# Kernel optimization log

Hardware: AMD Instinct MI355X
Metric: run time of the kernel (lower is better)

The kernel has to match this reference:

```python
import jax, jax.numpy as jnp
import numpy as np


def setup_inputs() -> dict:
    key = jax.random.key(0)
    ks = jax.random.split(key, 8)
    B, I, H = 4096, 2048, 2048
    C = I + H
    s = 1.0 / np.sqrt(C)
    return {
        "x": jax.random.normal(ks[0], (B, I), jnp.float32),
        "h": jax.random.normal(ks[1], (B, H), jnp.float32),
        "W_update": jax.random.normal(ks[2], (H, C), jnp.float32) * s,
        "b_update": jax.random.normal(ks[3], (H,), jnp.float32) * s,
        "W_select": jax.random.normal(ks[4], (H, C), jnp.float32) * s,
        "b_select": jax.random.normal(ks[5], (H,), jnp.float32) * s,
        "W_predict": jax.random.normal(ks[6], (H, C), jnp.float32) * s,
        "b_predict": jax.random.normal(ks[7], (H,), jnp.float32) * s,
    }


def reference(x, h, W_update, b_update, W_select, b_select, W_predict, b_predict):
    # combined = [x, h]  -> [B, I+H]
    combined = jnp.concatenate([x, h], axis=1)
    to_update = jax.nn.sigmoid(combined @ W_update.T + b_update)  # [B, H]
    to_select = jax.nn.sigmoid(combined @ W_select.T + b_select)  # [B, H]
    updated = h * to_update
    new_combined = jnp.concatenate([x, updated], axis=1)
    predictions = jnp.tanh(new_combined @ W_predict.T + b_predict)
    selected = predictions * to_select
    h_new = h * (1.0 - to_select) + selected
    return h_new
```

## Files before the change

### kernel.cpp

```cpp
#include <hip/hip_runtime.h>
#include <stdint.h>

#define IDIM 2048
#define HDIM 2048
#define CDIM 4096
#define BDIM 4096
#define KDIM 4096

typedef float f32x4 __attribute__((ext_vector_type(4)));
typedef short s16x8 __attribute__((ext_vector_type(8)));
typedef unsigned short u16;
typedef u16 u16x8 __attribute__((ext_vector_type(8)));

__device__ __forceinline__ u16 f2bf(float f) {
    union { float f; uint32_t u; } v; v.f = f;
    uint32_t r = v.u + 0x7fffu + ((v.u >> 16) & 1u);
    return (u16)(r >> 16);
}

__device__ __forceinline__ void gload_lds16(const void* g, void* l) {
    __builtin_amdgcn_global_load_lds(
        (__attribute__((address_space(1))) void*)g,
        (__attribute__((address_space(3))) void*)l,
        16, 0, 0);
}

__global__ void cvt_bf16_kernel(const float* __restrict__ src, u16* __restrict__ dst,
                                int ngroups) {
    int i = blockIdx.x * blockDim.x + threadIdx.x;
    if (i >= ngroups) return;
    const float4* s4 = (const float4*)src;
    float4 v0 = s4[2 * i], v1 = s4[2 * i + 1];
    u16x8 o;
    o[0] = f2bf(v0.x); o[1] = f2bf(v0.y); o[2] = f2bf(v0.z); o[3] = f2bf(v0.w);
    o[4] = f2bf(v1.x); o[5] = f2bf(v1.y); o[6] = f2bf(v1.z); o[7] = f2bf(v1.w);
    ((u16x8*)dst)[i] = o;
}

__global__ void pack_combined_kernel(const float* __restrict__ x, const float* __restrict__ h,
                                     u16* __restrict__ comb, u16* __restrict__ newc) {
    int i = blockIdx.x * blockDim.x + threadIdx.x;
    if (i >= BDIM * (CDIM / 8)) return;
    int b = i >> 9;
    int c = (i & 511) * 8;
    const float* src = (c < IDIM) ? (x + (size_t)b * IDIM + c)
                                  : (h + (size_t)b * HDIM + (c - IDIM));
    float4 v0 = ((const float4*)src)[0], v1 = ((const float4*)src)[1];
    u16x8 o;
    o[0] = f2bf(v0.x); o[1] = f2bf(v0.y); o[2] = f2bf(v0.z); o[3] = f2bf(v0.w);
    o[4] = f2bf(v1.x); o[5] = f2bf(v1.y); o[6] = f2bf(v1.z); o[7] = f2bf(v1.w);
    *(u16x8*)(comb + (size_t)b * CDIM + c) = o;
    if (c < IDIM) *(u16x8*)(newc + (size_t)b * CDIM + c) = o;
}

__global__ void gemm_bt1(const u16* __restrict__ A, const u16* __restrict__ Bm,
                         const float* __restrict__ h,
                         const float* __restrict__ bias0, const float* __restrict__ bias1,
                         float* __restrict__ Sout, u16* __restrict__ newc) {
    constexpr int BM = 128, BK = 64;
    const int tid  = threadIdx.x;
    const int lane = tid & 63;
    const int wave = tid >> 6;
    const int wr = wave >> 1, wc = wave & 1;
    const int bm = blockIdx.y * BM;
    const int bn = blockIdx.x * BM;

    __shared__ __align__(16) u16 lA[BM * BK];
    __shared__ __align__(16) u16 lB[BM * BK];

    f32x4 acc[4][4] = {};

    const int srow = wave * 32 + (lane >> 3);
    const int sg   = (lane & 7) ^ (lane >> 3);

    auto stage = [&](int k0) {
        #pragma unroll
        for (int i = 0; i < 4; ++i) {
            const int r = srow + i * 8;
            gload_lds16(A  + (size_t)(bm + r) * KDIM + k0 + sg * 8,
                        &lA[(wave * 32 + i * 8) * 64]);
            gload_lds16(Bm + (size_t)(bn + r) * KDIM + k0 + sg * 8,
                        &lB[(wave * 32 + i * 8) * 64]);
        }
    };

    stage(0);
    constexpr int NT = KDIM / BK;
    for (int kt = 0; kt < NT; ++kt) {
        __syncthreads();
        #pragma unroll
        for (int ks = 0; ks < 2; ++ks) {
            s16x8 af[4], bfr[4];
            #pragma unroll
            for (int m = 0; m < 4; ++m) {
                const int row = wr * 64 + m * 16 + (lane & 15);
                const int j   = ks * 4 + (lane >> 4);
                af[m] = *(const s16x8*)&lA[row * 64 + ((j ^ (row & 7)) << 3)];
            }
            #pragma unroll
            for (int n = 0; n < 4; ++n) {
                const int row = wc * 64 + n * 16 + (lane & 15);
                const int j   = ks * 4 + (lane >> 4);
                bfr[n] = *(const s16x8*)&lB[row * 64 + ((j ^ (row & 7)) << 3)];
            }
            #pragma unroll
            for (int m = 0; m < 4; ++m)
                #pragma unroll
                for (int n = 0; n < 4; ++n)
                    acc[m][n] = __builtin_amdgcn_mfma_f32_16x16x32_bf16(
                        af[m], bfr[n], acc[m][n], 0, 0, 0);
        }
        __syncthreads();
        if (kt + 1 < NT) stage((kt + 1) * BK);
    }

    #pragma unroll
    for (int m = 0; m < 4; ++m) {
        const int r0 = bm + wr * 64 + m * 16 + ((lane >> 4) << 2);
        #pragma unroll
        for (int n = 0; n < 4; ++n) {
            const int col = bn + wc * 64 + n * 16 + (lane & 15);
            #pragma unroll
            for (int j = 0; j < 4; ++j) {
                const int r = r0 + j;
                const float v = acc[m][n][j];
                const float bv = (col < HDIM) ? bias0[col] : bias1[col - HDIM];
                const float sgm = 1.0f / (1.0f + __expf(-(v + bv)));
                if (col < HDIM) {
                    const float hv = h[(size_t)r * HDIM + col];
                    newc[(size_t)r * CDIM + IDIM + col] = f2bf(hv * sgm);
                } else {
                    Sout[(size_t)r * HDIM + (col - HDIM)] = sgm;
                }
            }
        }
    }
}

__global__ void gemm_bt2(const u16* __restrict__ A, const u16* __restrict__ Bm,
                         const float* __restrict__ h,
                         const float* __restrict__ bias0,
                         float* __restrict__ Sout) {
    constexpr int BM = 128, BN = 64, BK = 64;
    const int tid  = threadIdx.x;
    const int lane = tid & 63;
    const int wave = tid >> 6;
    const int wr = wave >> 1, wc = wave & 1;
    const int bm = blockIdx.y * BM;
    const int bn = blockIdx.x * BN;

    __shared__ __align__(16) u16 lA[BM * BK];
    __shared__ __align__(16) u16 lB[BN * BK];

    f32x4 acc[4][2] = {};

    const int sg = (lane & 7) ^ (lane >> 3);

    auto stage = [&](int k0) {
        #pragma unroll
        for (int i = 0; i < 4; ++i) {
            const int r = wave * 32 + i * 8 + (lane >> 3);
            gload_lds16(A + (size_t)(bm + r) * KDIM + k0 + sg * 8,
                        &lA[(wave * 32 + i * 8) * 64]);
        }
        #pragma unroll
        for (int i = 0; i < 2; ++i) {
            const int r = wave * 16 + i * 8 + (lane >> 3);
            gload_lds16(Bm + (size_t)(bn + r) * KDIM + k0 + sg * 8,
                        &lB[(wave * 16 + i * 8) * 64]);
        }
    };

    stage(0);
    constexpr int NT = KDIM / BK;
    for (int kt = 0; kt < NT; ++kt) {
        __syncthreads();
        #pragma unroll
        for (int ks = 0; ks < 2; ++ks) {
            s16x8 af[4], bfr[2];
            #pragma unroll
            for (int m = 0; m < 4; ++m) {
                const int row = wr * 64 + m * 16 + (lane & 15);
                const int j   = ks * 4 + (lane >> 4);
                af[m] = *(const s16x8*)&lA[row * 64 + ((j ^ (row & 7)) << 3)];
            }
            #pragma unroll
            for (int n = 0; n < 2; ++n) {
                const int row = wc * 32 + n * 16 + (lane & 15);
                const int j   = ks * 4 + (lane >> 4);
                bfr[n] = *(const s16x8*)&lB[row * 64 + ((j ^ (row & 7)) << 3)];
            }
            #pragma unroll
            for (int m = 0; m < 4; ++m)
                #pragma unroll
                for (int n = 0; n < 2; ++n)
                    acc[m][n] = __builtin_amdgcn_mfma_f32_16x16x32_bf16(
                        af[m], bfr[n], acc[m][n], 0, 0, 0);
        }
        __syncthreads();
        if (kt + 1 < NT) stage((kt + 1) * BK);
    }

    #pragma unroll
    for (int m = 0; m < 4; ++m) {
        const int r0 = bm + wr * 64 + m * 16 + ((lane >> 4) << 2);
        #pragma unroll
        for (int n = 0; n < 2; ++n) {
            const int col = bn + wc * 32 + n * 16 + (lane & 15);
            #pragma unroll
            for (int j = 0; j < 4; ++j) {
                const int r = r0 + j;
                const float p = tanhf(acc[m][n][j] + bias0[col]);
                const size_t idx = (size_t)r * HDIM + col;
                const float s  = Sout[idx];
                const float hv = h[idx];
                Sout[idx] = hv * (1.0f - s) + p * s;
            }
        }
    }
}

extern "C" void kernel_launch(void* const* d_in, const int* in_sizes, int n_in,
                              void* d_out, int out_size, void* d_ws, size_t ws_size,
                              hipStream_t stream) {
    (void)in_sizes; (void)n_in; (void)out_size; (void)ws_size;
    const float* x  = (const float*)d_in[0];
    const float* h  = (const float*)d_in[1];
    const float* Wu = (const float*)d_in[2];
    const float* bu = (const float*)d_in[3];
    const float* Ws = (const float*)d_in[4];
    const float* bs = (const float*)d_in[5];
    const float* Wp = (const float*)d_in[6];
    const float* bp = (const float*)d_in[7];
    float* out = (float*)d_out;

    u16* comb  = (u16*)d_ws;
    u16* newc  = comb  + (size_t)BDIM * CDIM;
    u16* wpack = newc  + (size_t)BDIM * CDIM;
    u16* wpred = wpack + (size_t)2 * HDIM * CDIM;

    const int WG = 256;
    const int wgrp = (HDIM * CDIM) / 8;
    cvt_bf16_kernel<<<wgrp / WG, WG, 0, stream>>>(Wu, wpack, wgrp);
    cvt_bf16_kernel<<<wgrp / WG, WG, 0, stream>>>(Ws, wpack + (size_t)HDIM * CDIM, wgrp);
    cvt_bf16_kernel<<<wgrp / WG, WG, 0, stream>>>(Wp, wpred, wgrp);
    const int cgrp = (BDIM * CDIM) / 8;
    pack_combined_kernel<<<cgrp / WG, WG, 0, stream>>>(x, h, comb, newc);

    gemm_bt1<<<dim3(CDIM / 128, BDIM / 128), 256, 0, stream>>>(
        comb, wpack, h, bu, bs, out, newc);
    gemm_bt2<<<dim3(HDIM / 64, BDIM / 128), 256, 0, stream>>>(
        newc, wpred, h, bp, out);
}
```

Baseline: 286.8 us.

## Rewrite first GEMM as 256x256 double-buffered 8-wave pipelined kernel

Replaces the 128x128 single-buffered gate GEMM with a 256x256 tile, 512-thread kernel that double-buffers LDS and splits each k-tile into four phases. Each phase interleaves async global->LDS prefetch of the next tile with MFMA on quadrants, using explicit waitcnt, barriers and setprio. It aims to hide load latency and raise arithmetic intensity for the largest GEMM. In exchange it needs 128 KB of LDS per block and more registers, which limits occupancy, and the hand-tuned waitcnt values must match the issue order exactly.

```diff
diff --git a/kernel.cpp b/kernel.cpp
--- a/kernel.cpp
+++ b/kernel.cpp
@@ -53,85 +53,148 @@
     if (c < IDIM) *(u16x8*)(newc + (size_t)b * CDIM + c) = o;
 }
 
-__global__ void gemm_bt1(const u16* __restrict__ A, const u16* __restrict__ Bm,
-                         const float* __restrict__ h,
-                         const float* __restrict__ bias0, const float* __restrict__ bias1,
-                         float* __restrict__ Sout, u16* __restrict__ newc) {
-    constexpr int BM = 128, BK = 64;
+__global__ __launch_bounds__(512, 2) void gemm8p(
+        const u16* __restrict__ A, const u16* __restrict__ Bm,
+        const float* __restrict__ h,
+        const float* __restrict__ bias0, const float* __restrict__ bias1,
+        float* __restrict__ Sout, u16* __restrict__ newc) {
+    constexpr int NT = KDIM / 64;
+
     const int tid  = threadIdx.x;
     const int lane = tid & 63;
     const int wave = tid >> 6;
-    const int wr = wave >> 1, wc = wave & 1;
-    const int bm = blockIdx.y * BM;
-    const int bn = blockIdx.x * BM;
-
-    __shared__ __align__(16) u16 lA[BM * BK];
-    __shared__ __align__(16) u16 lB[BM * BK];
-
-    f32x4 acc[4][4] = {};
-
-    const int srow = wave * 32 + (lane >> 3);
-    const int sg   = (lane & 7) ^ (lane >> 3);
-
-    auto stage = [&](int k0) {
-        #pragma unroll
-        for (int i = 0; i < 4; ++i) {
-            const int r = srow + i * 8;
-            gload_lds16(A  + (size_t)(bm + r) * KDIM + k0 + sg * 8,
-                        &lA[(wave * 32 + i * 8) * 64]);
-            gload_lds16(Bm + (size_t)(bn + r) * KDIM + k0 + sg * 8,
-                        &lB[(wave * 32 + i * 8) * 64]);
-        }
-    };
-
-    stage(0);
-    constexpr int NT = KDIM / BK;
-    for (int kt = 0; kt < NT; ++kt) {
-        __syncthreads();
-        #pragma unroll
-        for (int ks = 0; ks < 2; ++ks) {
-            s16x8 af[4], bfr[4];
-            #pragma unroll
-            for (int m = 0; m < 4; ++m) {
-                const int row = wr * 64 + m * 16 + (lane & 15);
-                const int j   = ks * 4 + (lane >> 4);
-                af[m] = *(const s16x8*)&lA[row * 64 + ((j ^ (row & 7)) << 3)];
-            }
-            #pragma unroll
-            for (int n = 0; n < 4; ++n) {
-                const int row = wc * 64 + n * 16 + (lane & 15);
-                const int j   = ks * 4 + (lane >> 4);
-                bfr[n] = *(const s16x8*)&lB[row * 64 + ((j ^ (row & 7)) << 3)];
-            }
-            #pragma unroll
-            for (int m = 0; m < 4; ++m)
-                #pragma unroll
-                for (int n = 0; n < 4; ++n)
-                    acc[m][n] = __builtin_amdgcn_mfma_f32_16x16x32_bf16(
-                        af[m], bfr[n], acc[m][n], 0, 0, 0);
-        }
-        __syncthreads();
-        if (kt + 1 < NT) stage((kt + 1) * BK);
-    }
-
-    #pragma unroll
-    for (int m = 0; m < 4; ++m) {
-        const int r0 = bm + wr * 64 + m * 16 + ((lane >> 4) << 2);
-        #pragma unroll
-        for (int n = 0; n < 4; ++n) {
-            const int col = bn + wc * 64 + n * 16 + (lane & 15);
-            #pragma unroll
-            for (int j = 0; j < 4; ++j) {
-                const int r = r0 + j;
-                const float v = acc[m][n][j];
-                const float bv = (col < HDIM) ? bias0[col] : bias1[col - HDIM];
-                const float sgm = 1.0f / (1.0f + __expf(-(v + bv)));
-                if (col < HDIM) {
-                    const float hv = h[(size_t)r * HDIM + col];
-                    newc[(size_t)r * CDIM + IDIM + col] = f2bf(hv * sgm);
-                } else {
-                    Sout[(size_t)r * HDIM + (col - HDIM)] = sgm;
-                }
+    const int wr = wave >> 2, wc = wave & 3;
+    const int bm = blockIdx.y * 256;
+    const int bn = blockIdx.x * 256;
+
+    __shared__ __align__(16) u16 lA[2][256 * 64];
+    __shared__ __align__(16) u16 lB[2][256 * 64];
+
+    f32x4 acc[8][4] = {};
+    s16x8 af[4][2];
+    s16x8 bq[2][2][2];
+
+    const int srow = tid >> 3;
+    const int ssw  = ((tid & 7) ^ ((tid >> 3) & 7)) << 3;
+
+#define STAGE_A(NB, c, k0)                                                      \
+    gload_lds16(A + (size_t)(bm + (c) * 64 + srow) * KDIM + (k0) + ssw,         \
+                &lA[NB][((c) * 64 + wave * 8) * 64]);
+#define STAGE_B(NB, c, k0)                                                      \
+    gload_lds16(Bm + (size_t)(bn + (c) * 64 + srow) * KDIM + (k0) + ssw,        \
+                &lB[NB][((c) * 64 + wave * 8) * 64]);
+
+#define READ_A(BUF, QM)                                                         \
+    _Pragma("unroll") for (int fm = 0; fm < 4; ++fm) {                          \
+        const int row_ = wr * 64 + (QM) * 128 + fm * 16 + (lane & 15);          \
+        const int bo_ = row_ * 64; const int rx_ = row_ & 7;                    \
+        af[fm][0] = *(const s16x8*)&lA[BUF][bo_ + ((((lane >> 4)    ) ^ rx_) << 3)]; \
+        af[fm][1] = *(const s16x8*)&lA[BUF][bo_ + ((((lane >> 4) + 4) ^ rx_) << 3)]; \
+    }
+#define READ_B(BUF, QN)                                                         \
+    _Pragma("unroll") for (int nf = 0; nf < 2; ++nf) {                          \
+        const int row_ = wc * 32 + (QN) * 128 + nf * 16 + (lane & 15);          \
+        const int bo_ = row_ * 64; const int rx_ = row_ & 7;                    \
+        bq[QN][nf][0] = *(const s16x8*)&lB[BUF][bo_ + ((((lane >> 4)    ) ^ rx_) << 3)]; \
+        bq[QN][nf][1] = *(const s16x8*)&lB[BUF][bo_ + ((((lane >> 4) + 4) ^ rx_) << 3)]; \
+    }
+#define MFMA_QUAD(QM, QN)                                                       \
+    _Pragma("unroll") for (int ks = 0; ks < 2; ++ks)                            \
+    _Pragma("unroll") for (int fm = 0; fm < 4; ++fm)                            \
+    _Pragma("unroll") for (int nf = 0; nf < 2; ++nf)                            \
+        acc[(QM) * 4 + fm][(QN) * 2 + nf] =                                     \
+            __builtin_amdgcn_mfma_f32_16x16x32_bf16(                            \
+                af[fm][ks], bq[QN][nf][ks], acc[(QM) * 4 + fm][(QN) * 2 + nf], 0, 0, 0);
+#define PHASE_MID()                                                             \
+    __builtin_amdgcn_s_barrier();                                               \
+    asm volatile("s_waitcnt lgkmcnt(0)" ::: "memory");                          \
+    __builtin_amdgcn_sched_barrier(0);                                          \
+    __builtin_amdgcn_s_setprio(1);
+#define PHASE_END(W)                                                            \
+    __builtin_amdgcn_s_setprio(0);                                              \
+    asm volatile("s_waitcnt vmcnt(" #W ")" ::: "memory");                       \
+    __builtin_amdgcn_s_barrier();
+#define PHASE_END_NOWAIT()                                                      \
+    __builtin_amdgcn_s_setprio(0);                                              \
+    __builtin_amdgcn_s_barrier();
+
+#define KTILE(BUF, NB, KN, PF, W0, W1, W3)                                      \
+    {                                                                           \
+                 \
+        READ_A(BUF, 0)                                                          \
+        READ_B(BUF, 0)                                                          \
+        if (PF) { STAGE_A(NB, 0, KN); STAGE_A(NB, 1, KN); }                     \
+        asm volatile("s_waitcnt lgkmcnt(8)" ::: "memory");                      \
+        PHASE_MID();                                                            \
+        MFMA_QUAD(0, 0);                                                        \
+        PHASE_END(W0);                                                          \
+                          \
+        READ_B(BUF, 1)                                                          \
+        if (PF) { STAGE_B(NB, 0, KN); STAGE_B(NB, 1, KN); }                     \
+        PHASE_MID();                                                            \
+        MFMA_QUAD(0, 1);                                                        \
+        PHASE_END(W1);                                                          \
+                          \
+        READ_A(BUF, 1)                                                          \
+        if (PF) { STAGE_B(NB, 2, KN); STAGE_B(NB, 3, KN); }                     \
+        PHASE_MID();                                                            \
+        MFMA_QUAD(1, 1);                                                        \
+        PHASE_END_NOWAIT();                                                     \
+                              \
+        if (PF) { STAGE_A(NB, 2, KN); STAGE_A(NB, 3, KN); }                     \
+        PHASE_MID();                                                            \
+        MFMA_QUAD(1, 0);                                                        \
+        PHASE_END(W3);                                                          \
+    }
+
+    STAGE_A(0, 0, 0); STAGE_A(0, 1, 0);
+    STAGE_B(0, 0, 0); STAGE_B(0, 1, 0);
+    STAGE_B(0, 2, 0); STAGE_B(0, 3, 0);
+    STAGE_A(0, 2, 0); STAGE_A(0, 3, 0);
+    asm volatile("s_waitcnt vmcnt(4)" ::: "memory");
+    __builtin_amdgcn_s_barrier();
+
+    for (int kt = 0; kt < NT - 2; kt += 2) {
+        const int kn0 = (kt + 1) * 64;
+        const int kn1 = (kt + 2) * 64;
+        KTILE(0, 1, kn0, 1, 4, 4, 4);
+        KTILE(1, 0, kn1, 1, 4, 4, 4);
+    }
+    KTILE(0, 1, (NT - 1) * 64, 1, 4, 4, 4);
+    KTILE(1, 0, 0, 0, 2, 0, 0);
+
+#undef KTILE
+#undef READ_A
+#undef READ_B
+#undef MFMA_QUAD
+#undef PHASE_MID
+#undef PHASE_END
+#undef PHASE_END_NOWAIT
+#undef STAGE_A
+#undef STAGE_B
+
+    #pragma unroll
+    for (int qm = 0; qm < 2; ++qm)
+    #pragma unroll
+    for (int fm = 0; fm < 4; ++fm)
+    #pragma unroll
+    for (int qn = 0; qn < 2; ++qn)
+    #pragma unroll
+    for (int nf = 0; nf < 2; ++nf) {
+        const int r0  = bm + wr * 64 + qm * 128 + fm * 16 + ((lane >> 4) << 2);
+        const int col = bn + wc * 32 + qn * 128 + nf * 16 + (lane & 15);
+        const f32x4 a = acc[qm * 4 + fm][qn * 2 + nf];
+        #pragma unroll
+        for (int j = 0; j < 4; ++j) {
+            const int r = r0 + j;
+            const float v = a[j];
+            const float bv = (col < HDIM) ? bias0[col] : bias1[col - HDIM];
+            const float sgm = 1.0f / (1.0f + __expf(-(v + bv)));
+            if (col < HDIM) {
+                const float hv = h[(size_t)r * HDIM + col];
+                newc[(size_t)r * CDIM + IDIM + col] = f2bf(hv * sgm);
+            } else {
+                Sout[(size_t)r * HDIM + (col - HDIM)] = sgm;
             }
         }
     }
@@ -247,7 +310,7 @@
     const int cgrp = (BDIM * CDIM) / 8;
     pack_combined_kernel<<<cgrp / WG, WG, 0, stream>>>(x, h, comb, newc);
 
-    gemm_bt1<<<dim3(CDIM / 128, BDIM / 128), 256, 0, stream>>>(
+    gemm8p<<<dim3(CDIM / 256, BDIM / 256), 512, 0, stream>>>(
         comb, wpack, h, bu, bs, out, newc);
     gemm_bt2<<<dim3(HDIM / 64, BDIM / 128), 256, 0, stream>>>(
         newc, wpred, h, bp, out);
```

New measurement: 295.6 us. 1.03x slower.

## Merge prep conversions into one kernel, fuse Wp cast into GEMM1, retile GEMM2

Applied to the files above, without the earlier changes.

Merges the three weight-cast launches and the combined-pack launch into one prep kernel. The W_predict bf16 conversion moves into the tail of the first GEMM, with each block converting a slice after its epilogue. The second GEMM now runs 2 waves of 128 threads, each computing 64x64, with launch bounds for 3 blocks per CU. This cuts launch count and gives GEMM2 more MFMA work per LDS load, at the cost of extra tail work in GEMM1 and fewer waves per block in GEMM2.

```diff
diff --git a/kernel.cpp b/kernel.cpp
--- a/kernel.cpp
+++ b/kernel.cpp
@@ -18,6 +18,13 @@
     return (u16)(r >> 16);
 }
 
+__device__ __forceinline__ u16x8 cvt8(float4 v0, float4 v1) {
+    u16x8 o;
+    o[0] = f2bf(v0.x); o[1] = f2bf(v0.y); o[2] = f2bf(v0.z); o[3] = f2bf(v0.w);
+    o[4] = f2bf(v1.x); o[5] = f2bf(v1.y); o[6] = f2bf(v1.z); o[7] = f2bf(v1.w);
+    return o;
+}
+
 __device__ __forceinline__ void gload_lds16(const void* g, void* l) {
     __builtin_amdgcn_global_load_lds(
         (__attribute__((address_space(1))) void*)g,
@@ -25,38 +32,35 @@
         16, 0, 0);
 }
 
-__global__ void cvt_bf16_kernel(const float* __restrict__ src, u16* __restrict__ dst,
-                                int ngroups) {
+__global__ void prep_kernel(const float* __restrict__ x, const float* __restrict__ h,
+                            const float* __restrict__ Wu, const float* __restrict__ Ws,
+                            u16* __restrict__ comb, u16* __restrict__ newc,
+                            u16* __restrict__ wpack) {
+    const int WCNT = (HDIM * CDIM) / 8;
     int i = blockIdx.x * blockDim.x + threadIdx.x;
-    if (i >= ngroups) return;
-    const float4* s4 = (const float4*)src;
-    float4 v0 = s4[2 * i], v1 = s4[2 * i + 1];
-    u16x8 o;
-    o[0] = f2bf(v0.x); o[1] = f2bf(v0.y); o[2] = f2bf(v0.z); o[3] = f2bf(v0.w);
-    o[4] = f2bf(v1.x); o[5] = f2bf(v1.y); o[6] = f2bf(v1.z); o[7] = f2bf(v1.w);
-    ((u16x8*)dst)[i] = o;
-}
-
-__global__ void pack_combined_kernel(const float* __restrict__ x, const float* __restrict__ h,
-                                     u16* __restrict__ comb, u16* __restrict__ newc) {
-    int i = blockIdx.x * blockDim.x + threadIdx.x;
-    if (i >= BDIM * (CDIM / 8)) return;
-    int b = i >> 9;
-    int c = (i & 511) * 8;
-    const float* src = (c < IDIM) ? (x + (size_t)b * IDIM + c)
-                                  : (h + (size_t)b * HDIM + (c - IDIM));
-    float4 v0 = ((const float4*)src)[0], v1 = ((const float4*)src)[1];
-    u16x8 o;
-    o[0] = f2bf(v0.x); o[1] = f2bf(v0.y); o[2] = f2bf(v0.z); o[3] = f2bf(v0.w);
-    o[4] = f2bf(v1.x); o[5] = f2bf(v1.y); o[6] = f2bf(v1.z); o[7] = f2bf(v1.w);
-    *(u16x8*)(comb + (size_t)b * CDIM + c) = o;
-    if (c < IDIM) *(u16x8*)(newc + (size_t)b * CDIM + c) = o;
+    if (i < 2 * WCNT) {
+        const float* src = (i < WCNT) ? Wu : Ws;
+        const int g = (i < WCNT) ? i : i - WCNT;
+        u16* dst = wpack + (i < WCNT ? (size_t)0 : (size_t)HDIM * CDIM);
+        const float4* s4 = (const float4*)src;
+        ((u16x8*)dst)[g] = cvt8(s4[2 * g], s4[2 * g + 1]);
+    } else {
+        const int p = i - 2 * WCNT;
+        const int b = p >> 9;
+        const int c = (p & 511) * 8;
+        const float* src = (c < IDIM) ? (x + (size_t)b * IDIM + c)
+                                      : (h + (size_t)b * HDIM + (c - IDIM));
+        u16x8 o = cvt8(((const float4*)src)[0], ((const float4*)src)[1]);
+        *(u16x8*)(comb + (size_t)b * CDIM + c) = o;
+        if (c < IDIM) *(u16x8*)(newc + (size_t)b * CDIM + c) = o;
+    }
 }
 
 __global__ void gemm_bt1(const u16* __restrict__ A, const u16* __restrict__ Bm,
                          const float* __restrict__ h,
                          const float* __restrict__ bias0, const float* __restrict__ bias1,
-                         float* __restrict__ Sout, u16* __restrict__ newc) {
+                         float* __restrict__ Sout, u16* __restrict__ newc,
+                         const float* __restrict__ Wp, u16* __restrict__ wpred) {
     constexpr int BM = 128, BK = 64;
     const int tid  = threadIdx.x;
     const int lane = tid & 63;
@@ -135,40 +139,48 @@
             }
         }
     }
-}
-
-__global__ void gemm_bt2(const u16* __restrict__ A, const u16* __restrict__ Bm,
-                         const float* __restrict__ h,
-                         const float* __restrict__ bias0,
-                         float* __restrict__ Sout) {
+
+    {
+        const int bid = blockIdx.y * (CDIM / 128) + blockIdx.x;
+        const size_t base = (size_t)bid * 8192;
+        const float4* s4 = (const float4*)(Wp + base);
+        u16x8* d8 = (u16x8*)(wpred + base);
+        #pragma unroll
+        for (int t = 0; t < 4; ++t) {
+            const int g = t * 256 + tid;
+            d8[g] = cvt8(s4[2 * g], s4[2 * g + 1]);
+        }
+    }
+}
+
+__global__ __launch_bounds__(128, 3) void gemm_bt2(
+        const u16* __restrict__ A, const u16* __restrict__ Bm,
+        const float* __restrict__ h, const float* __restrict__ bias0,
+        float* __restrict__ Sout) {
     constexpr int BM = 128, BN = 64, BK = 64;
     const int tid  = threadIdx.x;
     const int lane = tid & 63;
     const int wave = tid >> 6;
-    const int wr = wave >> 1, wc = wave & 1;
     const int bm = blockIdx.y * BM;
     const int bn = blockIdx.x * BN;
 
     __shared__ __align__(16) u16 lA[BM * BK];
     __shared__ __align__(16) u16 lB[BN * BK];
 
-    f32x4 acc[4][2] = {};
-
-    const int sg = (lane & 7) ^ (lane >> 3);
+    f32x4 acc[4][4] = {};
+
+    const int srow = tid >> 3;
+    const int ssw  = ((tid & 7) ^ (srow & 7)) << 3;
 
     auto stage = [&](int k0) {
         #pragma unroll
-        for (int i = 0; i < 4; ++i) {
-            const int r = wave * 32 + i * 8 + (lane >> 3);
-            gload_lds16(A + (size_t)(bm + r) * KDIM + k0 + sg * 8,
-                        &lA[(wave * 32 + i * 8) * 64]);
-        }
-        #pragma unroll
-        for (int i = 0; i < 2; ++i) {
-            const int r = wave * 16 + i * 8 + (lane >> 3);
-            gload_lds16(Bm + (size_t)(bn + r) * KDIM + k0 + sg * 8,
-                        &lB[(wave * 16 + i * 8) * 64]);
-        }
+        for (int c = 0; c < 8; ++c)
+            gload_lds16(A + (size_t)(bm + c * 16 + srow) * KDIM + k0 + ssw,
+                        &lA[(c * 16 + wave * 8) * 64]);
+        #pragma unroll
+        for (int c = 0; c < 4; ++c)
+            gload_lds16(Bm + (size_t)(bn + c * 16 + srow) * KDIM + k0 + ssw,
+                        &lB[(c * 16 + wave * 8) * 64]);
     };
 
     stage(0);
@@ -177,23 +189,23 @@
         __syncthreads();
         #pragma unroll
         for (int ks = 0; ks < 2; ++ks) {
-            s16x8 af[4], bfr[2];
+            s16x8 af[4], bfr[4];
             #pragma unroll
             for (int m = 0; m < 4; ++m) {
-                const int row = wr * 64 + m * 16 + (lane & 15);
+                const int row = wave * 64 + m * 16 + (lane & 15);
                 const int j   = ks * 4 + (lane >> 4);
                 af[m] = *(const s16x8*)&lA[row * 64 + ((j ^ (row & 7)) << 3)];
             }
             #pragma unroll
-            for (int n = 0; n < 2; ++n) {
-                const int row = wc * 32 + n * 16 + (lane & 15);
+            for (int n = 0; n < 4; ++n) {
+                const int row = n * 16 + (lane & 15);
                 const int j   = ks * 4 + (lane >> 4);
                 bfr[n] = *(const s16x8*)&lB[row * 64 + ((j ^ (row & 7)) << 3)];
             }
             #pragma unroll
             for (int m = 0; m < 4; ++m)
                 #pragma unroll
-                for (int n = 0; n < 2; ++n)
+                for (int n = 0; n < 4; ++n)
                     acc[m][n] = __builtin_amdgcn_mfma_f32_16x16x32_bf16(
                         af[m], bfr[n], acc[m][n], 0, 0, 0);
         }
@@ -203,10 +215,10 @@
 
     #pragma unroll
     for (int m = 0; m < 4; ++m) {
-        const int r0 = bm + wr * 64 + m * 16 + ((lane >> 4) << 2);
-        #pragma unroll
-        for (int n = 0; n < 2; ++n) {
-            const int col = bn + wc * 32 + n * 16 + (lane & 15);
+        const int r0 = bm + wave * 64 + m * 16 + ((lane >> 4) << 2);
+        #pragma unroll
+        for (int n = 0; n < 4; ++n) {
+            const int col = bn + n * 16 + (lane & 15);
             #pragma unroll
             for (int j = 0; j < 4; ++j) {
                 const int r = r0 + j;
@@ -239,16 +251,11 @@
     u16* wpack = newc  + (size_t)BDIM * CDIM;
     u16* wpred = wpack + (size_t)2 * HDIM * CDIM;
 
-    const int WG = 256;
-    const int wgrp = (HDIM * CDIM) / 8;
-    cvt_bf16_kernel<<<wgrp / WG, WG, 0, stream>>>(Wu, wpack, wgrp);
-    cvt_bf16_kernel<<<wgrp / WG, WG, 0, stream>>>(Ws, wpack + (size_t)HDIM * CDIM, wgrp);
-    cvt_bf16_kernel<<<wgrp / WG, WG, 0, stream>>>(Wp, wpred, wgrp);
-    const int cgrp = (BDIM * CDIM) / 8;
-    pack_combined_kernel<<<cgrp / WG, WG, 0, stream>>>(x, h, comb, newc);
+    const int ngrp = 2 * ((HDIM * CDIM) / 8) + (BDIM * CDIM) / 8;
+    prep_kernel<<<ngrp / 256, 256, 0, stream>>>(x, h, Wu, Ws, comb, newc, wpack);
 
     gemm_bt1<<<dim3(CDIM / 128, BDIM / 128), 256, 0, stream>>>(
-        comb, wpack, h, bu, bs, out, newc);
-    gemm_bt2<<<dim3(HDIM / 64, BDIM / 128), 256, 0, stream>>>(
+        comb, wpack, h, bu, bs, out, newc, Wp, wpred);
+    gemm_bt2<<<dim3(HDIM / 64, BDIM / 128), 128, 0, stream>>>(
         newc, wpred, h, bp, out);
 }
```

Result: no change. 290.2 us (+1.2%).
